# Performance work log

Hardware: AMD Instinct MI355X
Metric: run time of the kernel (lower is better)

## Reference

```python
import jax, jax.numpy as jnp
import numpy as np

HIDDEN = 768
N_HEADS = 12
HEAD_DIM = HIDDEN // N_HEADS  # 64
SEQ = 2048
BATCH = 2
ROPE_BASE = 10000.0


def _rope_cos_sin(seq_len, head_dim):
    inv_freq = 1.0 / (ROPE_BASE ** (jnp.arange(0, head_dim, 2, dtype=jnp.float32) / head_dim))
    t = jnp.arange(seq_len, dtype=jnp.float32)
    freqs = jnp.einsum('s,d->sd', t, inv_freq)          # [S, D/2]
    emb = jnp.concatenate([freqs, freqs], axis=-1)      # [S, D]
    return jnp.cos(emb), jnp.sin(emb)


def _rotate_half(x):
    x1, x2 = jnp.split(x, 2, axis=-1)
    return jnp.concatenate([-x2, x1], axis=-1)


def setup_inputs() -> dict:
    key = jax.random.key(0)
    ks = jax.random.split(key, 6)
    scale = 1.0 / np.sqrt(HIDDEN)
    hidden_states = jax.random.normal(ks[0], (BATCH, SEQ, HIDDEN), dtype=jnp.float32)
    wq = jax.random.normal(ks[1], (HIDDEN, HIDDEN), dtype=jnp.float32) * scale
    wk = jax.random.normal(ks[2], (HIDDEN, HIDDEN), dtype=jnp.float32) * scale
    wv = jax.random.normal(ks[3], (HIDDEN, HIDDEN), dtype=jnp.float32) * scale
    wo = jax.random.normal(ks[4], (HIDDEN, HIDDEN), dtype=jnp.float32) * scale
    # additive causal mask: 0 on/below diagonal, large negative above
    causal = jnp.triu(jnp.full((SEQ, SEQ), -1e9, dtype=jnp.float32), k=1)
    attn_mask = causal[None, None, :, :]
    return {"hidden_states": hidden_states, "wq": wq, "wk": wk, "wv": wv,
            "wo": wo, "attn_mask": attn_mask}


def reference(hidden_states, wq, wk, wv, wo, attn_mask):
    B, S, _ = hidden_states.shape
    # projections (nn.Linear: x @ W.T)
    def proj(w):
        y = jnp.einsum('bsh,oh->bso', hidden_states, w)
        return y.reshape(B, S, N_HEADS, HEAD_DIM).transpose(0, 2, 1, 3)  # [B,H,S,D]
    q, k, v = proj(wq), proj(wk), proj(wv)
    cos, sin = _rope_cos_sin(S, HEAD_DIM)  # [S, D]
    cos = cos[None, None, :, :].astype(hidden_states.dtype)
    sin = sin[None, None, :, :].astype(hidden_states.dtype)
    q = q * cos + _rotate_half(q) * sin
    k = k * cos + _rotate_half(k) * sin
    scores = jnp.einsum('bhqd,bhkd->bhqk', q, k) / np.sqrt(HEAD_DIM)
    scores = scores + attn_mask
    probs = jax.nn.softmax(scores.astype(jnp.float32), axis=-1).astype(q.dtype)
    out = jnp.einsum('bhqk,bhkd->bhqd', probs, v)
    out = out.transpose(0, 2, 1, 3).reshape(B, S, HIDDEN)
    return jnp.einsum('bsh,oh->bso', out, wo)
```

## Files before the change

kernel.cpp:

```cpp
#include <hip/hip_runtime.h>

typedef unsigned short u16;
typedef short short8 __attribute__((ext_vector_type(8)));
typedef float f32x4 __attribute__((ext_vector_type(4)));

static_assert(sizeof(short8) == 16, "short8 must be 16B");

__device__ __forceinline__ u16 f2bf(float f) {
  unsigned u = __float_as_uint(f);
  u += 0x7FFFu + ((u >> 16) & 1u);
  return (u16)(u >> 16);
}
__device__ __forceinline__ float bf2f(u16 h) { return __uint_as_float(((unsigned)h) << 16); }

__device__ __forceinline__ f32x4 mfma_bf16(short8 a, short8 b, f32x4 c) {
  return __builtin_amdgcn_mfma_f32_16x16x32_bf16(a, b, c, 0, 0, 0);
}

__device__ __forceinline__ void gload_lds16(const void* g, void* l) {
  __builtin_amdgcn_global_load_lds((__attribute__((address_space(1))) void*)g,
                                   (__attribute__((address_space(3))) void*)l, 16, 0, 0);
}

__device__ __forceinline__ float exp2v(float x) {
  float r; asm("v_exp_f32 %0, %1" : "=v"(r) : "v"(x)); return r;
}
__device__ __forceinline__ unsigned cvtpk(float lo, float hi) {
  unsigned r; asm("v_cvt_pk_bf16_f32 %0, %1, %2" : "=v"(r) : "v"(lo), "v"(hi)); return r;
}
__device__ __forceinline__ f32x4 vmax4(f32x4 a, f32x4 b) {
  f32x4 r;
  r[0] = fmaxf(a[0], b[0]); r[1] = fmaxf(a[1], b[1]);
  r[2] = fmaxf(a[2], b[2]); r[3] = fmaxf(a[3], b[3]);
  return r;
}

__global__ __launch_bounds__(256) void cvt_kernel(
    const float* __restrict__ hs, const float* __restrict__ wq, const float* __restrict__ wk,
    const float* __restrict__ wv, const float* __restrict__ wo,
    u16* __restrict__ hbf, u16* __restrict__ wbf) {
  int i = blockIdx.x * 256 + threadIdx.x;
  const float* src; u16* dst; int idx;
  if (i < 786432) {
    src = hs; dst = hbf; idx = i;
  } else {
    int j = i - 786432;
    int seg = j / 147456;
    idx = j - seg * 147456;
    src = (seg == 0) ? wq : (seg == 1) ? wk : (seg == 2) ? wv : wo;
    dst = wbf + seg * 589824;
  }
  float4 v = ((const float4*)src)[idx];
  uint2 r;
  r.x = (unsigned)f2bf(v.x) | ((unsigned)f2bf(v.y) << 16);
  r.y = (unsigned)f2bf(v.z) | ((unsigned)f2bf(v.w) << 16);
  ((uint2*)dst)[idx] = r;
}

template <int MODE>
__global__ __launch_bounds__(256, 2) void gemm_bt(
    const u16* __restrict__ A, const u16* __restrict__ Bm,
    u16* __restrict__ qb, u16* __restrict__ kb, u16* __restrict__ vtb,
    float* __restrict__ fout) {
  __shared__ __align__(16) char sm[49152];
  const int K = 768, NK = 12;
  const int t = threadIdx.x;
  const int lane = t & 63;
  const int w = t >> 6;
  const int wr = w >> 1, wc = w & 1;
  const int lrow = lane & 15, lkg = lane >> 4;

  const int l = (MODE == 0) ? ((blockIdx.x & 7) * 144 + (blockIdx.x >> 3))
                            : ((blockIdx.x & 7) * 48 + (blockIdx.x >> 3));
  const int bx = (MODE == 0) ? (l / 18) : (l / 6);
  const int by = (MODE == 0) ? (l % 18) : (l % 6);
  const int arow0 = bx * 64, brow0 = by * 128;

  f32x4 acc[2][4];
  const f32x4 z4 = {0.f, 0.f, 0.f, 0.f};
#pragma unroll
  for (int m = 0; m < 2; ++m)
#pragma unroll
    for (int n = 0; n < 4; ++n) acc[m][n] = z4;

  const int srow = t >> 3;
  const int sslot = t & 7;

  auto STAGE = [&](int ki, int b) {
    char* sA = sm + b * 24576;
    char* sB = sA + 8192;
    const int kt = ki * 64;
#pragma unroll
    for (int it = 0; it < 2; ++it) {
      int r = it * 32 + srow;
      int ls = sslot ^ (r & 7);
      gload_lds16(A + (size_t)(arow0 + r) * K + (kt + ls * 8), sA + it * 4096 + w * 1024);
    }
#pragma unroll
    for (int it = 0; it < 4; ++it) {
      int r = it * 32 + srow;
      int ls = sslot ^ (r & 7);
      gload_lds16(Bm + (size_t)(brow0 + r) * K + (kt + ls * 8), sB + it * 4096 + w * 1024);
    }
  };

  STAGE(0, 0);
  __syncthreads();

  for (int ki = 0; ki < NK; ++ki) {
    const int cur = ki & 1;
    if (ki + 1 < NK) STAGE(ki + 1, cur ^ 1);
    const char* sA = sm + cur * 24576;
    const char* sB = sA + 8192;
#pragma unroll
    for (int kk = 0; kk < 2; ++kk) {
      short8 af[2], bfr[4];
#pragma unroll
      for (int m = 0; m < 2; ++m) {
        int row = wr * 32 + m * 16 + lrow;
        int ph = (kk * 4 + lkg) ^ (row & 7);
        af[m] = *(const short8*)(sA + row * 128 + ph * 16);
      }
#pragma unroll
      for (int n = 0; n < 4; ++n) {
        int row = wc * 64 + n * 16 + lrow;
        int ph = (kk * 4 + lkg) ^ (row & 7);
        bfr[n] = *(const short8*)(sB + row * 128 + ph * 16);
      }
#pragma unroll
      for (int m = 0; m < 2; ++m)
#pragma unroll
        for (int n = 0; n < 4; ++n) acc[m][n] = mfma_bf16(af[m], bfr[n], acc[m][n]);
    }
    __syncthreads();
  }

  if (MODE == 1) {
#pragma unroll
    for (int m = 0; m < 2; ++m)
#pragma unroll
      for (int n = 0; n < 4; ++n)
#pragma unroll
        for (int i = 0; i < 4; ++i) {
          int row = arow0 + wr * 32 + m * 16 + lkg * 4 + i;
          int col = brow0 + wc * 64 + n * 16 + lrow;
          fout[(size_t)row * 768 + col] = acc[m][n][i];
        }
  } else {
    const int qsel = brow0 / 768;
    if (qsel < 2) {
      u16* dst = qsel ? kb : qb;
      const float oscale = qsel ? 1.0f : 0.1803368801111244f;
      float fr[2];
      fr[0] = __expf(-0.2878231366242557f * (float)lrow);
      fr[1] = __expf(-0.2878231366242557f * (float)(16 + lrow));
      const int hh = ((brow0 - qsel * 768) >> 6) + wc;
#pragma unroll
      for (int m = 0; m < 2; ++m)
#pragma unroll
        for (int i = 0; i < 4; ++i) {
          int row = arow0 + wr * 32 + m * 16 + lkg * 4 + i;
          int b = row >> 11, s = row & 2047;
          size_t base = ((size_t)(b * 12 + hh) * 2048 + s) * 64;
#pragma unroll
          for (int n2 = 0; n2 < 2; ++n2) {
            float x1 = acc[m][n2][i], x2 = acc[m][n2 + 2][i];
            float th = (float)s * fr[n2];
            float sn, cs;
            __sincosf(th, &sn, &cs);
            dst[base + n2 * 16 + lrow]      = f2bf((x1 * cs - x2 * sn) * oscale);
            dst[base + 32 + n2 * 16 + lrow] = f2bf((x2 * cs + x1 * sn) * oscale);
          }
        }
    } else {
#pragma unroll
      for (int m = 0; m < 2; ++m)
#pragma unroll
        for (int n = 0; n < 4; ++n)
#pragma unroll
          for (int i = 0; i < 4; ++i) {
            int row = arow0 + wr * 32 + m * 16 + lkg * 4 + i;
            int col = brow0 + wc * 64 + n * 16 + lrow;
            int b = row >> 11, s = row & 2047;
            int oc = col - 1536, h = oc >> 6, d = oc & 63;
            vtb[((size_t)(b * 12 + h) * 64 + d) * 2048 + s] = f2bf(acc[m][n][i]);
          }
    }
  }
}

__global__ __launch_bounds__(256, 4) void attn_fwd(
    const u16* __restrict__ qg, const u16* __restrict__ kg,
    const u16* __restrict__ vtg, u16* __restrict__ og) {
  __shared__ __align__(16) char sm[32768];
  const int lane = threadIdx.x & 63;
  const int w = threadIdx.x >> 6;
  const int lrow = lane & 15, lkg = lane >> 4;

  const int u = blockIdx.x;
  const int xcd = u & 7, vv = u >> 3;
  const int bh = xcd * 3 + (vv % 3);
  const int qc = 31 - (vv / 3);
  const int qw = qc * 64 + w * 16;
  const int niter = qc + 1;

  const u16* Q  = qg  + (size_t)bh * (2048 * 64);
  const u16* Kp = kg  + (size_t)bh * (2048 * 64);
  const u16* VT = vtg + (size_t)bh * (64 * 2048);

  short8 qf[2];
#pragma unroll
  for (int h = 0; h < 2; ++h)
    qf[h] = *(const short8*)(Q + (size_t)(qw + lrow) * 64 + h * 32 + lkg * 8);

  const f32x4 z4 = {0.f, 0.f, 0.f, 0.f};
  f32x4 o[4] = {z4, z4, z4, z4};
  float m_ = -1e30f, l_ = 0.f;

  const int s_rl = lane >> 3;
  const int s_p  = lane & 7;
  auto STAGE = [&](int t, int b) {
    const int kv0 = t << 6;
    char* sk = sm + b * 16384;
    char* sv = sk + 8192;
    int r0 = w * 16 + s_rl, r1 = r0 + 8;
    gload_lds16(Kp + (size_t)(kv0 + r0) * 64 + ((s_p ^ (r0 & 7)) << 3), sk + w * 2048);
    gload_lds16(Kp + (size_t)(kv0 + r1) * 64 + ((s_p ^ (r1 & 7)) << 3), sk + w * 2048 + 1024);
    gload_lds16(VT + (size_t)r0 * 2048 + kv0 + ((s_p ^ (r0 & 7)) << 3), sv + w * 2048);
    gload_lds16(VT + (size_t)r1 * 2048 + kv0 + ((s_p ^ (r1 & 7)) << 3), sv + w * 2048 + 1024);
  };

  STAGE(0, 0);
  __syncthreads();

  for (int t = 0; t < niter; ++t) {
    const int kv0 = t << 6;
    const int cur = t & 1;
    if (t + 1 < niter) STAGE(t + 1, cur ^ 1);

    const char* sk = sm + cur * 16384;
    const char* sv = sk + 8192;

    f32x4 s[4];
    __builtin_amdgcn_s_setprio(1);
#pragma unroll
    for (int kb = 0; kb < 4; ++kb) {
      int r = kb * 16 + lrow, sw = r & 7;
      short8 kf0 = *(const short8*)(sk + r * 128 + ((lkg ^ sw) << 4));
      short8 kf1 = *(const short8*)(sk + r * 128 + (((4 + lkg) ^ sw) << 4));
      s[kb] = mfma_bf16(kf0, qf[0], z4);
      s[kb] = mfma_bf16(kf1, qf[1], s[kb]);
    }
    __builtin_amdgcn_s_setprio(0);

    if (t == qc) {
      int qa = qw + lrow;
#pragma unroll
      for (int kb = 0; kb < 4; ++kb)
#pragma unroll
        for (int i = 0; i < 4; ++i)
          if (kv0 + kb * 16 + lkg * 4 + i > qa) s[kb][i] = -1e30f;
    }

    f32x4 m03 = vmax4(vmax4(s[0], s[1]), vmax4(s[2], s[3]));
    float mt = fmaxf(fmaxf(m03[0], m03[1]), fmaxf(m03[2], m03[3]));
    mt = fmaxf(mt, __shfl_xor(mt, 16));
    mt = fmaxf(mt, __shfl_xor(mt, 32));
    if (__any(mt > m_ + 8.0f)) {
      float mn = fmaxf(m_, mt);
      float sclf = exp2v(m_ - mn);
      m_ = mn;
      l_ *= sclf;
      float sc0 = __shfl(sclf, lkg * 4 + 0);
      float sc1 = __shfl(sclf, lkg * 4 + 1);
      float sc2 = __shfl(sclf, lkg * 4 + 2);
      float sc3 = __shfl(sclf, lkg * 4 + 3);
#pragma unroll
      for (int db = 0; db < 4; ++db) {
        o[db][0] *= sc0; o[db][1] *= sc1; o[db][2] *= sc2; o[db][3] *= sc3;
      }
    }
#pragma unroll
    for (int kb = 0; kb < 4; ++kb)
#pragma unroll
      for (int i = 0; i < 4; ++i) s[kb][i] = exp2v(s[kb][i] - m_);
    f32x4 st = (s[0] + s[1]) + (s[2] + s[3]);
    l_ += (st[0] + st[1]) + (st[2] + st[3]);

    uint4 p0 = { cvtpk(s[0][0], s[0][1]), cvtpk(s[0][2], s[0][3]),
                 cvtpk(s[1][0], s[1][1]), cvtpk(s[1][2], s[1][3]) };
    uint4 p1 = { cvtpk(s[2][0], s[2][1]), cvtpk(s[2][2], s[2][3]),
                 cvtpk(s[3][0], s[3][1]), cvtpk(s[3][2], s[3][3]) };
    short8 pa0 = __builtin_bit_cast(short8, p0);
    short8 pa1 = __builtin_bit_cast(short8, p1);

    __builtin_amdgcn_s_setprio(1);
#pragma unroll
    for (int db = 0; db < 4; ++db) {
      int d = db * 16 + lrow, sw = d & 7;
#pragma unroll
      for (int hk = 0; hk < 2; ++hk) {
        int b1 = 64 * hk + 8 * lkg;
        int b2 = b1 + 32;
        uint2 va = *(const uint2*)(sv + d * 128 + ((((b1 >> 4) ^ sw) << 4) | (b1 & 15)));
        uint2 vb = *(const uint2*)(sv + d * 128 + ((((b2 >> 4) ^ sw) << 4) | (b2 & 15)));
        uint4 uu = {va.x, va.y, vb.x, vb.y};
        short8 vf = __builtin_bit_cast(short8, uu);
        o[db] = mfma_bf16(hk ? pa1 : pa0, vf, o[db]);
      }
    }
    __builtin_amdgcn_s_setprio(0);
    __syncthreads();
  }

  l_ += __shfl_xor(l_, 16);
  l_ += __shfl_xor(l_, 32);
  int b = bh / 12, h = bh - b * 12;
  float nn[4];
  nn[0] = 1.0f / __shfl(l_, lkg * 4 + 0);
  nn[1] = 1.0f / __shfl(l_, lkg * 4 + 1);
  nn[2] = 1.0f / __shfl(l_, lkg * 4 + 2);
  nn[3] = 1.0f / __shfl(l_, lkg * 4 + 3);
#pragma unroll
  for (int i = 0; i < 4; ++i) {
    int qr = qw + lkg * 4 + i;
    u16* orow = og + ((size_t)(b * 2048 + qr)) * 768 + h * 64 + lrow;
    orow[0]  = f2bf(o[0][i] * nn[i]);
    orow[16] = f2bf(o[1][i] * nn[i]);
    orow[32] = f2bf(o[2][i] * nn[i]);
    orow[48] = f2bf(o[3][i] * nn[i]);
  }
}

extern "C" void kernel_launch(void* const* d_in, const int* in_sizes, int n_in,
                              void* d_out, int out_size, void* d_ws, size_t ws_size,
                              hipStream_t stream) {
  const float* hs = (const float*)d_in[0];
  const float* wq = (const float*)d_in[1];
  const float* wk = (const float*)d_in[2];
  const float* wv = (const float*)d_in[3];
  const float* wo = (const float*)d_in[4];
  float* out = (float*)d_out;
  char* ws = (char*)d_ws;

  u16* hbf = (u16*)(ws);
  u16* wbf = (u16*)(ws + 6291456);
  u16* qb  = (u16*)(ws + 11010048);
  u16* kb  = (u16*)(ws + 17301504);
  u16* vtb = (u16*)(ws + 23592960);
  u16* ob  = (u16*)(ws + 29884416);

  cvt_kernel<<<dim3(5376), 256, 0, stream>>>(hs, wq, wk, wv, wo, hbf, wbf);
  gemm_bt<0><<<dim3(1152), 256, 0, stream>>>(hbf, wbf, qb, kb, vtb, nullptr);
  attn_fwd<<<dim3(768), 256, 0, stream>>>(qb, kb, vtb, ob);
  gemm_bt<1><<<dim3(384), 256, 0, stream>>>(ob, wbf + 1769472, nullptr, nullptr, nullptr, out);
}
```

Before: 81.61 us.

## Permute V^T sequence layout so attention V fragments load as single 16-byte reads

The QKV projection epilogue now writes V^T with a permutation of the sequence index inside each 32-element group. This lets the attention PV stage fetch each V fragment with one 16-byte LDS read, replacing two 8-byte reads plus a repack. LDS fragment addresses in both the GEMM and attention kernels are precomputed once as swizzled base offsets. The attention loop is unrolled by two so the double-buffer pointers are compile-time constants, and global staging pointers are hoisted. Correctness depends on the permutation matching the MFMA operand layout of the probability fragments.

Result: faster. 73.96 us (-9.4%).

```diff
diff --git a/kernel.cpp b/kernel.cpp
--- a/kernel.cpp
+++ b/kernel.cpp
@@ -104,6 +104,9 @@
     }
   };
 
+  const int g0 = lrow * 128 + ((lkg ^ (lrow & 7)) << 4);
+  const int g1 = g0 ^ 64;
+
   STAGE(0, 0);
   __syncthreads();
 
@@ -114,19 +117,14 @@
     const char* sB = sA + 8192;
 #pragma unroll
     for (int kk = 0; kk < 2; ++kk) {
+      const int go = kk ? g1 : g0;
       short8 af[2], bfr[4];
 #pragma unroll
-      for (int m = 0; m < 2; ++m) {
-        int row = wr * 32 + m * 16 + lrow;
-        int ph = (kk * 4 + lkg) ^ (row & 7);
-        af[m] = *(const short8*)(sA + row * 128 + ph * 16);
-      }
-#pragma unroll
-      for (int n = 0; n < 4; ++n) {
-        int row = wc * 64 + n * 16 + lrow;
-        int ph = (kk * 4 + lkg) ^ (row & 7);
-        bfr[n] = *(const short8*)(sB + row * 128 + ph * 16);
-      }
+      for (int m = 0; m < 2; ++m)
+        af[m] = *(const short8*)(sA + wr * 4096 + m * 2048 + go);
+#pragma unroll
+      for (int n = 0; n < 4; ++n)
+        bfr[n] = *(const short8*)(sB + wc * 8192 + n * 2048 + go);
 #pragma unroll
       for (int m = 0; m < 2; ++m)
 #pragma unroll
@@ -182,8 +180,11 @@
             int row = arow0 + wr * 32 + m * 16 + lkg * 4 + i;
             int col = brow0 + wc * 64 + n * 16 + lrow;
             int b = row >> 11, s = row & 2047;
+            int sc = s & 31;
+            int p = ((sc & 12) << 1) | ((sc & 16) >> 2) | (sc & 3);
+            int s2 = (s & ~31) | p;
             int oc = col - 1536, h = oc >> 6, d = oc & 63;
-            vtb[((size_t)(b * 12 + h) * 64 + d) * 2048 + s] = f2bf(acc[m][n][i]);
+            vtb[((size_t)(b * 12 + h) * 64 + d) * 2048 + s2] = f2bf(acc[m][n][i]);
           }
     }
   }
@@ -217,44 +218,41 @@
   f32x4 o[4] = {z4, z4, z4, z4};
   float m_ = -1e30f, l_ = 0.f;
 
-  const int s_rl = lane >> 3;
-  const int s_p  = lane & 7;
+  const int a0 = lrow * 128 + ((lkg ^ (lrow & 7)) << 4);
+  const int a1 = a0 ^ 64;
+
+  const int s_rl = lane >> 3, s_p = lane & 7;
+  const int r0 = w * 16 + s_rl, r1 = r0 + 8;
+  const int ls = s_p ^ (r0 & 7);
+  const u16* kq0 = Kp + r0 * 64 + ls * 8;
+  const u16* kq1 = Kp + r1 * 64 + ls * 8;
+  const u16* vq0 = VT + (size_t)r0 * 2048 + ls * 8;
+  const u16* vq1 = VT + (size_t)r1 * 2048 + ls * 8;
+  const int sdst = w * 2048;
+
   auto STAGE = [&](int t, int b) {
-    const int kv0 = t << 6;
     char* sk = sm + b * 16384;
-    char* sv = sk + 8192;
-    int r0 = w * 16 + s_rl, r1 = r0 + 8;
-    gload_lds16(Kp + (size_t)(kv0 + r0) * 64 + ((s_p ^ (r0 & 7)) << 3), sk + w * 2048);
-    gload_lds16(Kp + (size_t)(kv0 + r1) * 64 + ((s_p ^ (r1 & 7)) << 3), sk + w * 2048 + 1024);
-    gload_lds16(VT + (size_t)r0 * 2048 + kv0 + ((s_p ^ (r0 & 7)) << 3), sv + w * 2048);
-    gload_lds16(VT + (size_t)r1 * 2048 + kv0 + ((s_p ^ (r1 & 7)) << 3), sv + w * 2048 + 1024);
+    gload_lds16(kq0 + t * 4096, sk + sdst);
+    gload_lds16(kq1 + t * 4096, sk + sdst + 1024);
+    gload_lds16(vq0 + t * 64, sk + 8192 + sdst);
+    gload_lds16(vq1 + t * 64, sk + 8192 + sdst + 1024);
   };
 
-  STAGE(0, 0);
-  __syncthreads();
-
-  for (int t = 0; t < niter; ++t) {
-    const int kv0 = t << 6;
-    const int cur = t & 1;
-    if (t + 1 < niter) STAGE(t + 1, cur ^ 1);
-
-    const char* sk = sm + cur * 16384;
+  auto ITER = [&](int t, const char* sk) {
     const char* sv = sk + 8192;
-
     f32x4 s[4];
     __builtin_amdgcn_s_setprio(1);
 #pragma unroll
     for (int kb = 0; kb < 4; ++kb) {
-      int r = kb * 16 + lrow, sw = r & 7;
-      short8 kf0 = *(const short8*)(sk + r * 128 + ((lkg ^ sw) << 4));
-      short8 kf1 = *(const short8*)(sk + r * 128 + (((4 + lkg) ^ sw) << 4));
+      short8 kf0 = *(const short8*)(sk + kb * 2048 + a0);
+      short8 kf1 = *(const short8*)(sk + kb * 2048 + a1);
       s[kb] = mfma_bf16(kf0, qf[0], z4);
       s[kb] = mfma_bf16(kf1, qf[1], s[kb]);
     }
     __builtin_amdgcn_s_setprio(0);
 
-    if (t == qc) {
-      int qa = qw + lrow;
+    if (t == niter - 1) {
+      int qa = qw + lrow, kv0 = t << 6;
 #pragma unroll
       for (int kb = 0; kb < 4; ++kb)
 #pragma unroll
@@ -297,20 +295,27 @@
     __builtin_amdgcn_s_setprio(1);
 #pragma unroll
     for (int db = 0; db < 4; ++db) {
-      int d = db * 16 + lrow, sw = d & 7;
-#pragma unroll
-      for (int hk = 0; hk < 2; ++hk) {
-        int b1 = 64 * hk + 8 * lkg;
-        int b2 = b1 + 32;
-        uint2 va = *(const uint2*)(sv + d * 128 + ((((b1 >> 4) ^ sw) << 4) | (b1 & 15)));
-        uint2 vb = *(const uint2*)(sv + d * 128 + ((((b2 >> 4) ^ sw) << 4) | (b2 & 15)));
-        uint4 uu = {va.x, va.y, vb.x, vb.y};
-        short8 vf = __builtin_bit_cast(short8, uu);
-        o[db] = mfma_bf16(hk ? pa1 : pa0, vf, o[db]);
-      }
+      short8 vf0 = *(const short8*)(sv + db * 2048 + a0);
+      short8 vf1 = *(const short8*)(sv + db * 2048 + a1);
+      o[db] = mfma_bf16(pa0, vf0, o[db]);
+      o[db] = mfma_bf16(pa1, vf1, o[db]);
     }
     __builtin_amdgcn_s_setprio(0);
+  };
+
+  STAGE(0, 0);
+  __syncthreads();
+
+  int t = 0;
+  while (true) {
+    if (t + 1 < niter) STAGE(t + 1, 1);
+    ITER(t, sm);
     __syncthreads();
+    if (++t >= niter) break;
+    if (t + 1 < niter) STAGE(t + 1, 0);
+    ITER(t, sm + 16384);
+    __syncthreads();
+    if (++t >= niter) break;
   }
 
   l_ += __shfl_xor(l_, 16);
```
